# Optimization experiments

Hardware: AMD Instinct MI355X
Metric: run time of the kernel (lower is better)

The kernel has to match this reference:

```python
import jax, jax.numpy as jnp
import numpy as np


def _gcn_conv(X, src, dst, norm, W, n_nodes):
    # gather + normalized aggregate (SpMM) then dense linear (GEMM)
    msg = X[src] * norm[:, None]                       # [E, F]
    agg = jax.ops.segment_sum(msg, dst, num_segments=n_nodes)  # [N, F]
    return agg @ W                                     # [N, F_out]


def setup_inputs() -> dict:
    key = jax.random.key(0)
    k1, k2, k3, k4, k5 = jax.random.split(key, 5)
    N, E, D_IN, D_HID, D_OUT = 50000, 800000, 128, 128, 64
    X = jax.random.normal(k1, (N, D_IN), dtype=jnp.float32)
    edge_index = jax.random.randint(k2, (2, E), 0, N, dtype=jnp.int64)
    s = 1.0 / np.sqrt(D_IN)
    W1 = jax.random.normal(k3, (D_IN, D_HID), dtype=jnp.float32) * s
    W2 = jax.random.normal(k4, (D_HID, D_HID), dtype=jnp.float32) * s
    W3 = jax.random.normal(k5, (D_HID, D_OUT), dtype=jnp.float32) * s
    return {"X": X, "edge_index": edge_index, "W1": W1, "W2": W2, "W3": W3}


def reference(X, edge_index, W1, W2, W3):
    n_nodes = X.shape[0]
    src, dst = edge_index[0], edge_index[1]
    # symmetric degree normalization D^-1/2 A D^-1/2 (degrees from edge list)
    ones = jnp.ones(src.shape[0], dtype=X.dtype)
    deg = jax.ops.segment_sum(ones, dst, num_segments=n_nodes)
    deg = jnp.maximum(deg, 1.0)
    dinv = jax.lax.rsqrt(deg)
    norm = dinv[src] * dinv[dst]                       # [E]
    h = jax.nn.relu(_gcn_conv(X, src, dst, norm, W1, n_nodes))
    h = jax.nn.relu(_gcn_conv(h, src, dst, norm, W2, n_nodes))
    h = jax.nn.relu(_gcn_conv(h, src, dst, norm, W3, n_nodes))
    return jax.nn.softmax(h, axis=-1)
```

## Files before the change

kernel.cpp:

```cpp
#include <hip/hip_runtime.h>
#include <hip/hip_bf16.h>

typedef __attribute__((ext_vector_type(8))) short short8;
typedef __attribute__((ext_vector_type(4))) short short4v;
typedef __attribute__((ext_vector_type(4))) float f32x4;

static inline size_t ws_align(size_t x) { return (x + 511) & ~((size_t)511); }

static __device__ inline unsigned short f2bf(float f) {
    __hip_bfloat16 h = __float2bfloat16(f);
    return __builtin_bit_cast(unsigned short, h);
}
static __device__ inline float bfbits2f(unsigned short u) {
    unsigned x = ((unsigned)u) << 16;
    return __builtin_bit_cast(float, x);
}

static __device__ inline int sniff_fp32(const unsigned short* __restrict__ w1) {
    int i = threadIdx.x & 63;
    unsigned e = (w1[2 * i] >> 7) & 0xFF;
    unsigned long long m = __ballot(e >= 100 && e <= 130);
    return (__popcll(m) < 48) ? 1 : 0;
}
static __device__ inline int sniff_is64(const unsigned int* __restrict__ ei) {
    int i = threadIdx.x & 63;
    unsigned long long m = __ballot(ei[2 * i + 1] == 0u);
    return (__popcll(m) >= 48) ? 1 : 0;
}

__global__ void hist_kernel(const int* __restrict__ ei,
                            int* __restrict__ counts, int* __restrict__ loff, int E) {
    int is64 = sniff_is64((const unsigned int*)ei);
    int e = blockIdx.x * blockDim.x + threadIdx.x;
    if (e < E) {
        int d = is64 ? ei[2 * (size_t)E + 2 * e] : ei[(size_t)E + e];
        loff[e] = atomicAdd(&counts[d], 1);
    }
}

__global__ __launch_bounds__(256) void alloc_kernel(const int* __restrict__ counts,
                                                    float* __restrict__ dinv,
                                                    int2* __restrict__ rc,
                                                    int* __restrict__ total, int N) {
    int n = blockIdx.x * blockDim.x + threadIdx.x;
    int lane = threadIdx.x & 63;
    int c = (n < N) ? counts[n] : 0;
    if (n < N) {
        int d = (c < 1) ? 1 : c;
        dinv[n] = rsqrtf((float)d);
    }
    int lenp = (c + 7) & ~7;
    int incl = lenp;
#pragma unroll
    for (int off = 1; off < 64; off <<= 1) {
        int v = __shfl_up(incl, off, 64);
        if (lane >= off) incl += v;
    }
    int wavetot = __shfl(incl, 63, 64);
    int base = 0;
    if (lane == 0) base = atomicAdd(total, wavetot);
    base = __shfl(base, 0, 64);
    if (n < N) rc[n] = make_int2(base + incl - lenp, lenp);
}

__global__ void fill_kernel(const int* __restrict__ ei,
                            const float* __restrict__ dinv, const int2* __restrict__ rc,
                            const int* __restrict__ loff, int2* __restrict__ edgedat, int E) {
    int is64 = sniff_is64((const unsigned int*)ei);
    int e = blockIdx.x * blockDim.x + threadIdx.x;
    if (e < E) {
        int s, d;
        if (is64) {
            s = ei[2 * e];
            d = ei[2 * (size_t)E + 2 * e];
        } else {
            s = ei[e];
            d = ei[(size_t)E + e];
        }
        int pos = rc[d].x + loff[e];
        float wt = dinv[s] * dinv[d];
        edgedat[pos] = make_int2(s, __float_as_int(wt));
    }
}


template <int FOUT>
__global__ __launch_bounds__(256) void gemm_kernel(const void* __restrict__ Araw, int a_follows,
                                                   const void* __restrict__ Wraw,
                                                   const unsigned short* __restrict__ w1sniff,
                                                   unsigned short* __restrict__ out, int Nrows) {
    constexpr int K = 128;
    constexpr int NT = FOUT / 16;
    constexpr int LDB = K + 8;
    __shared__ __align__(16) unsigned short bt[FOUT * LDB];

    const int tid = threadIdx.x;
    const int in_fp32 = sniff_fp32(w1sniff);
    const int a_fp32 = a_follows & in_fp32;

    constexpr int TOT4 = K * FOUT / 4;
    if (in_fp32) {
        const float* Wf = (const float*)Wraw;
        for (int i = tid; i < TOT4; i += 256) {
            int idx = i * 4;
            int k = idx / FOUT;
            int n = idx & (FOUT - 1);
            float4 v = *(const float4*)(const void*)(Wf + idx);
            bt[(n + 0) * LDB + k] = f2bf(v.x);
            bt[(n + 1) * LDB + k] = f2bf(v.y);
            bt[(n + 2) * LDB + k] = f2bf(v.z);
            bt[(n + 3) * LDB + k] = f2bf(v.w);
        }
    } else {
        const unsigned short* Ws = (const unsigned short*)Wraw;
        for (int i = tid; i < TOT4; i += 256) {
            int idx = i * 4;
            int k = idx / FOUT;
            int n = idx & (FOUT - 1);
            short4v v = *(const short4v*)(const void*)(Ws + idx);
#pragma unroll
            for (int j = 0; j < 4; j++) bt[(n + j) * LDB + k] = ((const unsigned short*)&v)[j];
        }
    }

    const int wave = tid >> 6;
    const int lane = tid & 63;
    const int quad = lane >> 4;
    const int r16 = lane & 15;

    short8 afrag[2][4];
#pragma unroll
    for (int t = 0; t < 2; t++) {
        int arow = blockIdx.x * 128 + t * 64 + wave * 16 + r16;
        if (arow > Nrows - 1) arow = Nrows - 1;
        if (a_fp32) {
            const float* Ap = (const float*)Araw + (size_t)arow * K + quad * 8;
#pragma unroll
            for (int kk = 0; kk < 4; kk++) {
                float4 f0 = *(const float4*)(const void*)(Ap + kk * 32);
                float4 f1 = *(const float4*)(const void*)(Ap + kk * 32 + 4);
                short8 r;
                r[0] = (short)f2bf(f0.x); r[1] = (short)f2bf(f0.y);
                r[2] = (short)f2bf(f0.z); r[3] = (short)f2bf(f0.w);
                r[4] = (short)f2bf(f1.x); r[5] = (short)f2bf(f1.y);
                r[6] = (short)f2bf(f1.z); r[7] = (short)f2bf(f1.w);
                afrag[t][kk] = r;
            }
        } else {
            const unsigned short* Ap = (const unsigned short*)Araw + (size_t)arow * K + quad * 8;
#pragma unroll
            for (int kk = 0; kk < 4; kk++) afrag[t][kk] = *(const short8*)(const void*)(Ap + kk * 32);
        }
    }

    __syncthreads();

    f32x4 acc[2][NT];
#pragma unroll
    for (int t = 0; t < 2; t++)
#pragma unroll
        for (int nt = 0; nt < NT; nt++) acc[t][nt] = (f32x4){0.f, 0.f, 0.f, 0.f};

#pragma unroll
    for (int kk = 0; kk < 4; kk++) {
#pragma unroll
        for (int nt = 0; nt < NT; nt++) {
            short8 b = *(const short8*)(const void*)(&bt[(nt * 16 + r16) * LDB + kk * 32 + quad * 8]);
#pragma unroll
            for (int t = 0; t < 2; t++)
                acc[t][nt] = __builtin_amdgcn_mfma_f32_16x16x32_bf16(afrag[t][kk], b, acc[t][nt], 0, 0, 0);
        }
    }

#pragma unroll
    for (int t = 0; t < 2; t++) {
#pragma unroll
        for (int nt = 0; nt < NT; nt++) {
#pragma unroll
            for (int r = 0; r < 4; r++) {
                float v = acc[t][nt][r];
                float o = __shfl_xor(v, 1, 64);
                int row = blockIdx.x * 128 + t * 64 + wave * 16 + quad * 4 + r;
                if (((lane & 1) == 0) && row < Nrows) {
                    __hip_bfloat162 pk;
                    pk.x = __float2bfloat16(v);
                    pk.y = __float2bfloat16(o);
                    *(__hip_bfloat162*)(out + (size_t)row * FOUT + nt * 16 + r16) = pk;
                }
            }
        }
    }
}


__global__ __launch_bounds__(256) void spmm128_kernel(const int2* __restrict__ edgedat,
                                                      const int2* __restrict__ rc,
                                                      const __hip_bfloat162* __restrict__ Hin,
                                                      __hip_bfloat162* __restrict__ Hout, int N) {
    int wid = (blockIdx.x * 256 + threadIdx.x) >> 6;
    if (wid >= N) return;
    int lane = threadIdx.x & 63;
    int2 r_ = rc[wid];
    int start = __builtin_amdgcn_readfirstlane(r_.x);
    int lenp  = __builtin_amdgcn_readfirstlane(r_.y);
    const __hip_bfloat162* col = Hin + lane;

    float ax = 0.f, ay = 0.f;
    for (int j = 0; j < lenp; j += 8) {
        int2 ed[8];
#pragma unroll
        for (int u = 0; u < 8; u++) ed[u] = edgedat[start + j + u];
        __hip_bfloat162 hv[8];
#pragma unroll
        for (int u = 0; u < 8; u++) hv[u] = col[(size_t)ed[u].x * 64];
#pragma unroll
        for (int u = 0; u < 8; u++) {
            float w = __int_as_float(ed[u].y);
            ax += w * __bfloat162float(hv[u].x);
            ay += w * __bfloat162float(hv[u].y);
        }
    }
    __hip_bfloat162 pk;
    pk.x = __float2bfloat16(fmaxf(ax, 0.f));
    pk.y = __float2bfloat16(fmaxf(ay, 0.f));
    Hout[(size_t)wid * 64 + lane] = pk;
}

__global__ __launch_bounds__(256) void spmm64_softmax_kernel(const int2* __restrict__ edgedat,
                                                             const int2* __restrict__ rc,
                                                             const unsigned short* __restrict__ Hin,
                                                             const unsigned short* __restrict__ w1sniff,
                                                             void* __restrict__ Out, int N) {
    int out_fp32 = sniff_fp32(w1sniff);
    int wid = (blockIdx.x * 256 + threadIdx.x) >> 6;
    if (wid >= N) return;
    int lane = threadIdx.x & 63;
    int2 r_ = rc[wid];
    int start = __builtin_amdgcn_readfirstlane(r_.x);
    int lenp  = __builtin_amdgcn_readfirstlane(r_.y);
    const unsigned short* col = Hin + lane;

    float a = 0.f;
    for (int j = 0; j < lenp; j += 8) {
        int2 ed[8];
#pragma unroll
        for (int u = 0; u < 8; u++) ed[u] = edgedat[start + j + u];
        float hv[8];
#pragma unroll
        for (int u = 0; u < 8; u++) hv[u] = bfbits2f(col[(size_t)ed[u].x * 64]);
#pragma unroll
        for (int u = 0; u < 8; u++) a += __int_as_float(ed[u].y) * hv[u];
    }
    a = fmaxf(a, 0.f);
    float m = a;
#pragma unroll
    for (int off = 32; off > 0; off >>= 1) m = fmaxf(m, __shfl_xor(m, off, 64));
    float e = __expf(a - m);
    float s = e;
#pragma unroll
    for (int off = 32; off > 0; off >>= 1) s += __shfl_xor(s, off, 64);
    float r = e / s;
    if (out_fp32) {
        ((float*)Out)[(size_t)wid * 64 + lane] = r;
    } else {
        ((unsigned short*)Out)[(size_t)wid * 64 + lane] = f2bf(r);
    }
}


extern "C" void kernel_launch(void* const* d_in, const int* in_sizes, int n_in,
                              void* d_out, int out_size, void* d_ws, size_t ws_size,
                              hipStream_t stream) {
    const void* X  = d_in[0];
    const int*  ei = (const int*)d_in[1];
    const void* W1 = d_in[2];
    const void* W2 = d_in[3];
    const void* W3 = d_in[4];
    const unsigned short* W1s = (const unsigned short*)W1;

    const int N = in_sizes[0] / 128;
    const int E = in_sizes[1] / 2;

    const size_t edgecap = (size_t)E + 8 * (size_t)N + 64;

    char* ws = (char*)d_ws;
    size_t off = 0;
    int* counts = (int*)(ws + off);   off += ws_align((size_t)N * 4);
    int* total  = (int*)(ws + off);   off += ws_align(64);
    const size_t zero_bytes = off;
    int2* rc      = (int2*)(ws + off);  off += ws_align((size_t)N * 8);
    float* dinv   = (float*)(ws + off); off += ws_align((size_t)N * 4);
    int* loff     = (int*)(ws + off);   off += ws_align((size_t)E * 4);
    int2* edgedat = (int2*)(ws + off);  off += ws_align(edgecap * 8);
    unsigned short* HA = (unsigned short*)(ws + off); off += ws_align((size_t)N * 128 * 2);
    unsigned short* HB = (unsigned short*)(ws + off); off += ws_align((size_t)N * 128 * 2);

    hipMemsetAsync(d_ws, 0, zero_bytes, stream);
    hipMemsetAsync(edgedat, 0, edgecap * 8, stream);

    hist_kernel<<<(E + 255) / 256, 256, 0, stream>>>(ei, counts, loff, E);
    alloc_kernel<<<(N + 255) / 256, 256, 0, stream>>>(counts, dinv, rc, total, N);
    fill_kernel<<<(E + 255) / 256, 256, 0, stream>>>(ei, dinv, rc, loff, edgedat, E);

    const int gblocks = (N + 127) / 128;
    const int sblocks = ((size_t)N * 64 + 255) / 256;

    gemm_kernel<128><<<gblocks, 256, 0, stream>>>(X, 1, W1, W1s, HA, N);
    spmm128_kernel<<<sblocks, 256, 0, stream>>>(edgedat, rc, (const __hip_bfloat162*)HA,
                                                (__hip_bfloat162*)HB, N);
    gemm_kernel<128><<<gblocks, 256, 0, stream>>>(HB, 0, W2, W1s, HA, N);
    spmm128_kernel<<<sblocks, 256, 0, stream>>>(edgedat, rc, (const __hip_bfloat162*)HA,
                                                (__hip_bfloat162*)HB, N);
    gemm_kernel<64><<<gblocks, 256, 0, stream>>>(HB, 0, W3, W1s, HA, N);
    spmm64_softmax_kernel<<<sblocks, 256, 0, stream>>>(edgedat, rc, HA, W1s, d_out, N);
}
```

Before: 274.7 us.

## Merge first GEMM with degree histogram and unroll SpMM edge loop to 16

The first dense GEMM (X@W1) and the degree-histogram pass now run in one launch, with blocks split by blockIdx, so the independent work overlaps and one launch is saved. Separately, per-row edge lists are padded to multiples of 16 instead of 8, and the SpMM gather loops are unrolled 16-wide for more memory-level parallelism per wave. The wider padding adds zero-weight padded edges (more wasted gathers at average degree 16), and the larger unroll raises register use.

```diff
diff --git a/kernel.cpp b/kernel.cpp
--- a/kernel.cpp
+++ b/kernel.cpp
@@ -28,13 +28,139 @@
     return (__popcll(m) >= 48) ? 1 : 0;
 }
 
-__global__ void hist_kernel(const int* __restrict__ ei,
-                            int* __restrict__ counts, int* __restrict__ loff, int E) {
-    int is64 = sniff_is64((const unsigned int*)ei);
-    int e = blockIdx.x * blockDim.x + threadIdx.x;
-    if (e < E) {
-        int d = is64 ? ei[2 * (size_t)E + 2 * e] : ei[(size_t)E + e];
-        loff[e] = atomicAdd(&counts[d], 1);
+
+template <int FOUT>
+static __device__ void gemm_body(const void* __restrict__ Araw, int a_follows,
+                                 const void* __restrict__ Wraw,
+                                 const unsigned short* __restrict__ w1sniff,
+                                 unsigned short* __restrict__ out, int Nrows, int bid) {
+    constexpr int K = 128;
+    constexpr int NT = FOUT / 16;
+    constexpr int LDB = K + 8;
+    __shared__ __align__(16) unsigned short bt[FOUT * LDB];
+
+    const int tid = threadIdx.x;
+    const int in_fp32 = sniff_fp32(w1sniff);
+    const int a_fp32 = a_follows & in_fp32;
+
+    constexpr int TOT4 = K * FOUT / 4;
+    if (in_fp32) {
+        const float* Wf = (const float*)Wraw;
+        for (int i = tid; i < TOT4; i += 256) {
+            int idx = i * 4;
+            int k = idx / FOUT;
+            int n = idx & (FOUT - 1);
+            float4 v = *(const float4*)(const void*)(Wf + idx);
+            bt[(n + 0) * LDB + k] = f2bf(v.x);
+            bt[(n + 1) * LDB + k] = f2bf(v.y);
+            bt[(n + 2) * LDB + k] = f2bf(v.z);
+            bt[(n + 3) * LDB + k] = f2bf(v.w);
+        }
+    } else {
+        const unsigned short* Ws = (const unsigned short*)Wraw;
+        for (int i = tid; i < TOT4; i += 256) {
+            int idx = i * 4;
+            int k = idx / FOUT;
+            int n = idx & (FOUT - 1);
+            short4v v = *(const short4v*)(const void*)(Ws + idx);
+#pragma unroll
+            for (int j = 0; j < 4; j++) bt[(n + j) * LDB + k] = ((const unsigned short*)&v)[j];
+        }
+    }
+
+    const int wave = tid >> 6;
+    const int lane = tid & 63;
+    const int quad = lane >> 4;
+    const int r16 = lane & 15;
+
+    short8 afrag[2][4];
+#pragma unroll
+    for (int t = 0; t < 2; t++) {
+        int arow = bid * 128 + t * 64 + wave * 16 + r16;
+        if (arow > Nrows - 1) arow = Nrows - 1;
+        if (a_fp32) {
+            const float* Ap = (const float*)Araw + (size_t)arow * K + quad * 8;
+#pragma unroll
+            for (int kk = 0; kk < 4; kk++) {
+                float4 f0 = *(const float4*)(const void*)(Ap + kk * 32);
+                float4 f1 = *(const float4*)(const void*)(Ap + kk * 32 + 4);
+                short8 r;
+                r[0] = (short)f2bf(f0.x); r[1] = (short)f2bf(f0.y);
+                r[2] = (short)f2bf(f0.z); r[3] = (short)f2bf(f0.w);
+                r[4] = (short)f2bf(f1.x); r[5] = (short)f2bf(f1.y);
+                r[6] = (short)f2bf(f1.z); r[7] = (short)f2bf(f1.w);
+                afrag[t][kk] = r;
+            }
+        } else {
+            const unsigned short* Ap = (const unsigned short*)Araw + (size_t)arow * K + quad * 8;
+#pragma unroll
+            for (int kk = 0; kk < 4; kk++) afrag[t][kk] = *(const short8*)(const void*)(Ap + kk * 32);
+        }
+    }
+
+    __syncthreads();
+
+    f32x4 acc[2][NT];
+#pragma unroll
+    for (int t = 0; t < 2; t++)
+#pragma unroll
+        for (int nt = 0; nt < NT; nt++) acc[t][nt] = (f32x4){0.f, 0.f, 0.f, 0.f};
+
+#pragma unroll
+    for (int kk = 0; kk < 4; kk++) {
+#pragma unroll
+        for (int nt = 0; nt < NT; nt++) {
+            short8 b = *(const short8*)(const void*)(&bt[(nt * 16 + r16) * LDB + kk * 32 + quad * 8]);
+#pragma unroll
+            for (int t = 0; t < 2; t++)
+                acc[t][nt] = __builtin_amdgcn_mfma_f32_16x16x32_bf16(afrag[t][kk], b, acc[t][nt], 0, 0, 0);
+        }
+    }
+
+#pragma unroll
+    for (int t = 0; t < 2; t++) {
+#pragma unroll
+        for (int nt = 0; nt < NT; nt++) {
+#pragma unroll
+            for (int r = 0; r < 4; r++) {
+                float v = acc[t][nt][r];
+                float o = __shfl_xor(v, 1, 64);
+                int row = bid * 128 + t * 64 + wave * 16 + quad * 4 + r;
+                if (((lane & 1) == 0) && row < Nrows) {
+                    __hip_bfloat162 pk;
+                    pk.x = __float2bfloat16(v);
+                    pk.y = __float2bfloat16(o);
+                    *(__hip_bfloat162*)(out + (size_t)row * FOUT + nt * 16 + r16) = pk;
+                }
+            }
+        }
+    }
+}
+
+template <int FOUT>
+__global__ __launch_bounds__(256) void gemm_kernel(const void* __restrict__ Araw, int a_follows,
+                                                   const void* __restrict__ Wraw,
+                                                   const unsigned short* __restrict__ w1sniff,
+                                                   unsigned short* __restrict__ out, int Nrows) {
+    gemm_body<FOUT>(Araw, a_follows, Wraw, w1sniff, out, Nrows, blockIdx.x);
+}
+
+__global__ __launch_bounds__(256) void gemm1_hist_kernel(const void* __restrict__ X,
+                                                         const void* __restrict__ W1,
+                                                         const unsigned short* __restrict__ w1sniff,
+                                                         unsigned short* __restrict__ HA, int N,
+                                                         const int* __restrict__ ei,
+                                                         int* __restrict__ counts,
+                                                         int* __restrict__ loff, int E, int gblocks) {
+    if ((int)blockIdx.x < gblocks) {
+        gemm_body<128>(X, 1, W1, w1sniff, HA, N, blockIdx.x);
+    } else {
+        int is64 = sniff_is64((const unsigned int*)ei);
+        int e = ((int)blockIdx.x - gblocks) * 256 + threadIdx.x;
+        if (e < E) {
+            int d = is64 ? ei[2 * (size_t)E + 2 * e] : ei[(size_t)E + e];
+            loff[e] = atomicAdd(&counts[d], 1);
+        }
     }
 }
 
@@ -49,7 +175,7 @@
         int d = (c < 1) ? 1 : c;
         dinv[n] = rsqrtf((float)d);
     }
-    int lenp = (c + 7) & ~7;
+    int lenp = (c + 15) & ~15;
     int incl = lenp;
 #pragma unroll
     for (int off = 1; off < 64; off <<= 1) {
@@ -84,115 +210,6 @@
 }
 
 
-template <int FOUT>
-__global__ __launch_bounds__(256) void gemm_kernel(const void* __restrict__ Araw, int a_follows,
-                                                   const void* __restrict__ Wraw,
-                                                   const unsigned short* __restrict__ w1sniff,
-                                                   unsigned short* __restrict__ out, int Nrows) {
-    constexpr int K = 128;
-    constexpr int NT = FOUT / 16;
-    constexpr int LDB = K + 8;
-    __shared__ __align__(16) unsigned short bt[FOUT * LDB];
-
-    const int tid = threadIdx.x;
-    const int in_fp32 = sniff_fp32(w1sniff);
-    const int a_fp32 = a_follows & in_fp32;
-
-    constexpr int TOT4 = K * FOUT / 4;
-    if (in_fp32) {
-        const float* Wf = (const float*)Wraw;
-        for (int i = tid; i < TOT4; i += 256) {
-            int idx = i * 4;
-            int k = idx / FOUT;
-            int n = idx & (FOUT - 1);
-            float4 v = *(const float4*)(const void*)(Wf + idx);
-            bt[(n + 0) * LDB + k] = f2bf(v.x);
-            bt[(n + 1) * LDB + k] = f2bf(v.y);
-            bt[(n + 2) * LDB + k] = f2bf(v.z);
-            bt[(n + 3) * LDB + k] = f2bf(v.w);
-        }
-    } else {
-        const unsigned short* Ws = (const unsigned short*)Wraw;
-        for (int i = tid; i < TOT4; i += 256) {
-            int idx = i * 4;
-            int k = idx / FOUT;
-            int n = idx & (FOUT - 1);
-            short4v v = *(const short4v*)(const void*)(Ws + idx);
-#pragma unroll
-            for (int j = 0; j < 4; j++) bt[(n + j) * LDB + k] = ((const unsigned short*)&v)[j];
-        }
-    }
-
-    const int wave = tid >> 6;
-    const int lane = tid & 63;
-    const int quad = lane >> 4;
-    const int r16 = lane & 15;
-
-    short8 afrag[2][4];
-#pragma unroll
-    for (int t = 0; t < 2; t++) {
-        int arow = blockIdx.x * 128 + t * 64 + wave * 16 + r16;
-        if (arow > Nrows - 1) arow = Nrows - 1;
-        if (a_fp32) {
-            const float* Ap = (const float*)Araw + (size_t)arow * K + quad * 8;
-#pragma unroll
-            for (int kk = 0; kk < 4; kk++) {
-                float4 f0 = *(const float4*)(const void*)(Ap + kk * 32);
-                float4 f1 = *(const float4*)(const void*)(Ap + kk * 32 + 4);
-                short8 r;
-                r[0] = (short)f2bf(f0.x); r[1] = (short)f2bf(f0.y);
-                r[2] = (short)f2bf(f0.z); r[3] = (short)f2bf(f0.w);
-                r[4] = (short)f2bf(f1.x); r[5] = (short)f2bf(f1.y);
-                r[6] = (short)f2bf(f1.z); r[7] = (short)f2bf(f1.w);
-                afrag[t][kk] = r;
-            }
-        } else {
-            const unsigned short* Ap = (const unsigned short*)Araw + (size_t)arow * K + quad * 8;
-#pragma unroll
-            for (int kk = 0; kk < 4; kk++) afrag[t][kk] = *(const short8*)(const void*)(Ap + kk * 32);
-        }
-    }
-
-    __syncthreads();
-
-    f32x4 acc[2][NT];
-#pragma unroll
-    for (int t = 0; t < 2; t++)
-#pragma unroll
-        for (int nt = 0; nt < NT; nt++) acc[t][nt] = (f32x4){0.f, 0.f, 0.f, 0.f};
-
-#pragma unroll
-    for (int kk = 0; kk < 4; kk++) {
-#pragma unroll
-        for (int nt = 0; nt < NT; nt++) {
-            short8 b = *(const short8*)(const void*)(&bt[(nt * 16 + r16) * LDB + kk * 32 + quad * 8]);
-#pragma unroll
-            for (int t = 0; t < 2; t++)
-                acc[t][nt] = __builtin_amdgcn_mfma_f32_16x16x32_bf16(afrag[t][kk], b, acc[t][nt], 0, 0, 0);
-        }
-    }
-
-#pragma unroll
-    for (int t = 0; t < 2; t++) {
-#pragma unroll
-        for (int nt = 0; nt < NT; nt++) {
-#pragma unroll
-            for (int r = 0; r < 4; r++) {
-                float v = acc[t][nt][r];
-                float o = __shfl_xor(v, 1, 64);
-                int row = blockIdx.x * 128 + t * 64 + wave * 16 + quad * 4 + r;
-                if (((lane & 1) == 0) && row < Nrows) {
-                    __hip_bfloat162 pk;
-                    pk.x = __float2bfloat16(v);
-                    pk.y = __float2bfloat16(o);
-                    *(__hip_bfloat162*)(out + (size_t)row * FOUT + nt * 16 + r16) = pk;
-                }
-            }
-        }
-    }
-}
-
-
 __global__ __launch_bounds__(256) void spmm128_kernel(const int2* __restrict__ edgedat,
                                                       const int2* __restrict__ rc,
                                                       const __hip_bfloat162* __restrict__ Hin,
@@ -206,15 +223,15 @@
     const __hip_bfloat162* col = Hin + lane;
 
     float ax = 0.f, ay = 0.f;
-    for (int j = 0; j < lenp; j += 8) {
-        int2 ed[8];
-#pragma unroll
-        for (int u = 0; u < 8; u++) ed[u] = edgedat[start + j + u];
-        __hip_bfloat162 hv[8];
-#pragma unroll
-        for (int u = 0; u < 8; u++) hv[u] = col[(size_t)ed[u].x * 64];
-#pragma unroll
-        for (int u = 0; u < 8; u++) {
+    for (int j = 0; j < lenp; j += 16) {
+        int2 ed[16];
+#pragma unroll
+        for (int u = 0; u < 16; u++) ed[u] = edgedat[start + j + u];
+        __hip_bfloat162 hv[16];
+#pragma unroll
+        for (int u = 0; u < 16; u++) hv[u] = col[(size_t)ed[u].x * 64];
+#pragma unroll
+        for (int u = 0; u < 16; u++) {
             float w = __int_as_float(ed[u].y);
             ax += w * __bfloat162float(hv[u].x);
             ay += w * __bfloat162float(hv[u].y);
@@ -241,15 +258,15 @@
     const unsigned short* col = Hin + lane;
 
     float a = 0.f;
-    for (int j = 0; j < lenp; j += 8) {
-        int2 ed[8];
-#pragma unroll
-        for (int u = 0; u < 8; u++) ed[u] = edgedat[start + j + u];
-        float hv[8];
-#pragma unroll
-        for (int u = 0; u < 8; u++) hv[u] = bfbits2f(col[(size_t)ed[u].x * 64]);
-#pragma unroll
-        for (int u = 0; u < 8; u++) a += __int_as_float(ed[u].y) * hv[u];
+    for (int j = 0; j < lenp; j += 16) {
+        int2 ed[16];
+#pragma unroll
+        for (int u = 0; u < 16; u++) ed[u] = edgedat[start + j + u];
+        float hv[16];
+#pragma unroll
+        for (int u = 0; u < 16; u++) hv[u] = bfbits2f(col[(size_t)ed[u].x * 64]);
+#pragma unroll
+        for (int u = 0; u < 16; u++) a += __int_as_float(ed[u].y) * hv[u];
     }
     a = fmaxf(a, 0.f);
     float m = a;
@@ -281,7 +298,7 @@
     const int N = in_sizes[0] / 128;
     const int E = in_sizes[1] / 2;
 
-    const size_t edgecap = (size_t)E + 8 * (size_t)N + 64;
+    const size_t edgecap = (size_t)E + 16 * (size_t)N + 64;
 
     char* ws = (char*)d_ws;
     size_t off = 0;
@@ -298,14 +315,15 @@
     hipMemsetAsync(d_ws, 0, zero_bytes, stream);
     hipMemsetAsync(edgedat, 0, edgecap * 8, stream);
 
-    hist_kernel<<<(E + 255) / 256, 256, 0, stream>>>(ei, counts, loff, E);
+    const int gblocks = (N + 127) / 128;
+    const int hblocks = (E + 255) / 256;
+    const int sblocks = ((size_t)N * 64 + 255) / 256;
+
+    gemm1_hist_kernel<<<gblocks + hblocks, 256, 0, stream>>>(X, W1, W1s, HA, N,
+                                                             ei, counts, loff, E, gblocks);
     alloc_kernel<<<(N + 255) / 256, 256, 0, stream>>>(counts, dinv, rc, total, N);
-    fill_kernel<<<(E + 255) / 256, 256, 0, stream>>>(ei, dinv, rc, loff, edgedat, E);
-
-    const int gblocks = (N + 127) / 128;
-    const int sblocks = ((size_t)N * 64 + 255) / 256;
-
-    gemm_kernel<128><<<gblocks, 256, 0, stream>>>(X, 1, W1, W1s, HA, N);
+    fill_kernel<<<hblocks, 256, 0, stream>>>(ei, dinv, rc, loff, edgedat, E);
+
     spmm128_kernel<<<sblocks, 256, 0, stream>>>(edgedat, rc, (const __hip_bfloat162*)HA,
                                                 (__hip_bfloat162*)HB, N);
     gemm_kernel<128><<<gblocks, 256, 0, stream>>>(HB, 0, W2, W1s, HA, N);
```

Measured after the change: 273.0 us. No clear change (-0.6%).

## Zero CSR padding in alloc kernel and split SpMM128 into two column halves

Applied to the files above, without the earlier changes.

Replaces the full memset of the edge array with per-node zeroing of only the padding slots inside alloc_kernel, removing a large memset pass over the edge buffer. The 128-wide SpMM now has each lane handle one bf16 per pass over two column halves instead of a bf16 pair, so the edge list is re-read twice and the gathers become 2-byte loads. This may reduce memset cost but increases edge-list traffic and load count in the SpMM.

```diff
diff --git a/kernel.cpp b/kernel.cpp
--- a/kernel.cpp
+++ b/kernel.cpp
@@ -41,6 +41,7 @@
 __global__ __launch_bounds__(256) void alloc_kernel(const int* __restrict__ counts,
                                                     float* __restrict__ dinv,
                                                     int2* __restrict__ rc,
+                                                    int2* __restrict__ edgedat,
                                                     int* __restrict__ total, int N) {
     int n = blockIdx.x * blockDim.x + threadIdx.x;
     int lane = threadIdx.x & 63;
@@ -60,7 +61,11 @@
     int base = 0;
     if (lane == 0) base = atomicAdd(total, wavetot);
     base = __shfl(base, 0, 64);
-    if (n < N) rc[n] = make_int2(base + incl - lenp, lenp);
+    if (n < N) {
+        int start = base + incl - lenp;
+        rc[n] = make_int2(start, lenp);
+        for (int p = c; p < lenp; p++) edgedat[start + p] = make_int2(0, 0);
+    }
 }
 
 __global__ void fill_kernel(const int* __restrict__ ei,
@@ -83,7 +88,6 @@
     }
 }
 
-
 template <int FOUT>
 __global__ __launch_bounds__(256) void gemm_kernel(const void* __restrict__ Araw, int a_follows,
                                                    const void* __restrict__ Wraw,
@@ -192,38 +196,33 @@
     }
 }
 
-
 __global__ __launch_bounds__(256) void spmm128_kernel(const int2* __restrict__ edgedat,
                                                       const int2* __restrict__ rc,
-                                                      const __hip_bfloat162* __restrict__ Hin,
-                                                      __hip_bfloat162* __restrict__ Hout, int N) {
+                                                      const unsigned short* __restrict__ Hin,
+                                                      unsigned short* __restrict__ Hout, int N) {
     int wid = (blockIdx.x * 256 + threadIdx.x) >> 6;
     if (wid >= N) return;
     int lane = threadIdx.x & 63;
     int2 r_ = rc[wid];
     int start = __builtin_amdgcn_readfirstlane(r_.x);
     int lenp  = __builtin_amdgcn_readfirstlane(r_.y);
-    const __hip_bfloat162* col = Hin + lane;
-
-    float ax = 0.f, ay = 0.f;
-    for (int j = 0; j < lenp; j += 8) {
-        int2 ed[8];
-#pragma unroll
-        for (int u = 0; u < 8; u++) ed[u] = edgedat[start + j + u];
-        __hip_bfloat162 hv[8];
-#pragma unroll
-        for (int u = 0; u < 8; u++) hv[u] = col[(size_t)ed[u].x * 64];
-#pragma unroll
-        for (int u = 0; u < 8; u++) {
-            float w = __int_as_float(ed[u].y);
-            ax += w * __bfloat162float(hv[u].x);
-            ay += w * __bfloat162float(hv[u].y);
-        }
-    }
-    __hip_bfloat162 pk;
-    pk.x = __float2bfloat16(fmaxf(ax, 0.f));
-    pk.y = __float2bfloat16(fmaxf(ay, 0.f));
-    Hout[(size_t)wid * 64 + lane] = pk;
+
+#pragma unroll
+    for (int p = 0; p < 2; p++) {
+        const unsigned short* col = Hin + p * 64 + lane;
+        float a = 0.f;
+        for (int j = 0; j < lenp; j += 8) {
+            int2 ed[8];
+#pragma unroll
+            for (int u = 0; u < 8; u++) ed[u] = edgedat[start + j + u];
+            float hv[8];
+#pragma unroll
+            for (int u = 0; u < 8; u++) hv[u] = bfbits2f(col[(size_t)ed[u].x * 128]);
+#pragma unroll
+            for (int u = 0; u < 8; u++) a += __int_as_float(ed[u].y) * hv[u];
+        }
+        Hout[(size_t)wid * 128 + p * 64 + lane] = f2bf(fmaxf(a, 0.f));
+    }
 }
 
 __global__ __launch_bounds__(256) void spmm64_softmax_kernel(const int2* __restrict__ edgedat,
@@ -267,7 +266,6 @@
     }
 }
 
-
 extern "C" void kernel_launch(void* const* d_in, const int* in_sizes, int n_in,
                               void* d_out, int out_size, void* d_ws, size_t ws_size,
                               hipStream_t stream) {
@@ -296,21 +294,18 @@
     unsigned short* HB = (unsigned short*)(ws + off); off += ws_align((size_t)N * 128 * 2);
 
     hipMemsetAsync(d_ws, 0, zero_bytes, stream);
-    hipMemsetAsync(edgedat, 0, edgecap * 8, stream);
 
     hist_kernel<<<(E + 255) / 256, 256, 0, stream>>>(ei, counts, loff, E);
-    alloc_kernel<<<(N + 255) / 256, 256, 0, stream>>>(counts, dinv, rc, total, N);
+    alloc_kernel<<<(N + 255) / 256, 256, 0, stream>>>(counts, dinv, rc, edgedat, total, N);
     fill_kernel<<<(E + 255) / 256, 256, 0, stream>>>(ei, dinv, rc, loff, edgedat, E);
 
     const int gblocks = (N + 127) / 128;
     const int sblocks = ((size_t)N * 64 + 255) / 256;
 
     gemm_kernel<128><<<gblocks, 256, 0, stream>>>(X, 1, W1, W1s, HA, N);
-    spmm128_kernel<<<sblocks, 256, 0, stream>>>(edgedat, rc, (const __hip_bfloat162*)HA,
-                                                (__hip_bfloat162*)HB, N);
+    spmm128_kernel<<<sblocks, 256, 0, stream>>>(edgedat, rc, HA, HB, N);
     gemm_kernel<128><<<gblocks, 256, 0, stream>>>(HB, 0, W2, W1s, HA, N);
-    spmm128_kernel<<<sblocks, 256, 0, stream>>>(edgedat, rc, (const __hip_bfloat162*)HA,
-                                                (__hip_bfloat162*)HB, N);
+    spmm128_kernel<<<sblocks, 256, 0, stream>>>(edgedat, rc, HA, HB, N);
     gemm_kernel<64><<<gblocks, 256, 0, stream>>>(HB, 0, W3, W1s, HA, N);
     spmm64_softmax_kernel<<<sblocks, 256, 0, stream>>>(edgedat, rc, HA, W1s, d_out, N);
 }
```

Result: slower. 284.1 us (+3.4%).
